# Kernel tuning notes

Hardware: AMD Instinct MI355X
Metric: run time of the kernel (lower is better)

The kernel has to match this reference:

```python
import jax, jax.numpy as jnp
import numpy as np

NUM_HEADS = 4


def setup_inputs() -> dict:
    key = jax.random.key(0)
    ks = jax.random.split(key, 5)
    B, C, L = 8, 128, 2048
    x = jax.random.normal(ks[0], (B, C, L), dtype=jnp.float32)
    # Conv1d(C, 3C, 1) == per-position linear; weight [3C, C], bias [3C]
    w_qkv = jax.random.normal(ks[1], (3 * C, C), dtype=jnp.float32) * (1.0 / np.sqrt(C))
    b_qkv = jax.random.normal(ks[2], (3 * C,), dtype=jnp.float32) * 0.01
    w_proj = jax.random.normal(ks[3], (C, C), dtype=jnp.float32) * (1.0 / np.sqrt(C))
    b_proj = jax.random.normal(ks[4], (C,), dtype=jnp.float32) * 0.01
    return {"x": x, "w_qkv": w_qkv, "b_qkv": b_qkv, "w_proj": w_proj, "b_proj": b_proj}


def reference(x, w_qkv, b_qkv, w_proj, b_proj):
    B, C, L = x.shape
    H = NUM_HEADS
    D = C // H
    scale = D ** -0.5
    # 1x1 conv qkv projection: [B, 3C, L]
    qkv = jnp.einsum('oc,bcl->bol', w_qkv, x) + b_qkv[None, :, None]
    # reshape (B,3,H,D,L) -> permute to (3,B,H,L,D)
    qkv = qkv.reshape(B, 3, H, D, L).transpose(1, 0, 2, 4, 3)
    q, k, v = qkv[0], qkv[1], qkv[2]  # each [B, H, L, D]
    attn = jax.nn.softmax(jnp.einsum('bhld,bhmd->bhlm', q, k) * scale, axis=-1)
    out = jnp.einsum('bhlm,bhmd->bhld', attn, v)  # [B, H, L, D]
    out = out.transpose(0, 1, 3, 2).reshape(B, C, L)
    out = jnp.einsum('oc,bcl->bol', w_proj, out) + b_proj[None, :, None]
    return out + x
```

## Files before the change

### kernel.cpp

```cpp
#include <hip/hip_runtime.h>

#define Bsz 8
#define Cdim 128
#define Lseq 2048
#define NH 4
#define HD 32
#define BH 32
#define QSCALE (0.17677669529663687f * 1.4426950408889634f)

typedef __bf16 bf16x8 __attribute__((ext_vector_type(8)));
typedef float f32x4 __attribute__((ext_vector_type(4)));
typedef unsigned u32x4 __attribute__((ext_vector_type(4)));

__device__ __forceinline__ float fexp2(float x) {
#if __has_builtin(__builtin_amdgcn_exp2f)
    return __builtin_amdgcn_exp2f(x);
#else
    return __expf(x * 0.6931471805599453f);
#endif
}

__device__ __forceinline__ unsigned short f2bf(float f) {
    unsigned u = __builtin_bit_cast(unsigned, f);
    u += 0x7FFFu + ((u >> 16) & 1u);
    return (unsigned short)(u >> 16);
}

__device__ __forceinline__ unsigned pack_bf16(float a, float b) {
    return (unsigned)f2bf(a) | ((unsigned)f2bf(b) << 16);
}

__device__ __forceinline__ unsigned pack_bf16_rtz(float a, float b) {
    return __builtin_amdgcn_perm(__builtin_bit_cast(unsigned, b),
                                 __builtin_bit_cast(unsigned, a), 0x07060302u);
}

__device__ __forceinline__ float bf_lo(unsigned u) {
    return __builtin_bit_cast(float, u << 16);
}
__device__ __forceinline__ float bf_hi(unsigned u) {
    return __builtin_bit_cast(float, u & 0xFFFF0000u);
}

#define MFMA16(A, B, C) __builtin_amdgcn_mfma_f32_16x16x32_bf16((A), (B), (C), 0, 0, 0)

__global__ __launch_bounds__(256) void qkv_kernel(const float* __restrict__ x,
        const float* __restrict__ w, const float* __restrict__ bias,
        unsigned short* __restrict__ qh, unsigned short* __restrict__ kh,
        unsigned short* __restrict__ vh) {
    __shared__ __attribute__((aligned(16))) unsigned short T[64][132];
    int bid = blockIdx.x;
    int og = bid % 6;
    int lt = (bid / 6) & 31;
    int b  = bid / 192;
    int l0 = lt * 64;
    int t = threadIdx.x;
    int lane = t & 63, wv = t >> 6;
    int m16 = lane & 15, quad = lane >> 4;
    int o0 = og * 64 + wv * 16;

    bf16x8 af[4];
    #pragma unroll
    for (int ks = 0; ks < 4; ks++) {
        const float* p = w + (size_t)(o0 + m16) * Cdim + ks * 32 + quad * 8;
        float4 f0 = *(const float4*)p;
        float4 f1 = *(const float4*)(p + 4);
        u32x4 u = {pack_bf16(f0.x, f0.y), pack_bf16(f0.z, f0.w),
                   pack_bf16(f1.x, f1.y), pack_bf16(f1.z, f1.w)};
        af[ks] = __builtin_bit_cast(bf16x8, u);
    }
    float bs[4];
    #pragma unroll
    for (int r = 0; r < 4; r++) bs[r] = bias[o0 + quad * 4 + r];

    {
        int ll = t & 63, cg = t >> 6;
        const float* xb = x + (size_t)b * Cdim * Lseq + l0 + ll;
        #pragma unroll
        for (int i = 0; i < 16; i++) {
            int c = cg * 32 + 2 * i;
            float f0 = xb[(size_t)c * Lseq];
            float f1 = xb[(size_t)(c + 1) * Lseq];
            *(unsigned*)&T[ll][c] = pack_bf16(f0, f1);
        }
    }
    __syncthreads();

    int oq = o0 + quad * 4;
    #pragma unroll
    for (int ns = 0; ns < 4; ns++) {
        bf16x8 bx[4];
        #pragma unroll
        for (int ks = 0; ks < 4; ks++)
            bx[ks] = *(const bf16x8*)(&T[ns * 16 + m16][ks * 32 + quad * 8]);
        f32x4 acc = {0.f, 0.f, 0.f, 0.f};
        #pragma unroll
        for (int ks = 0; ks < 4; ks++) acc = MFMA16(af[ks], bx[ks], acc);
        int l = l0 + ns * 16 + m16;
        if (og < 2) {
            int h = oq >> 5, d0 = oq & 31;
            uint2 u;
            u.x = pack_bf16((acc[0] + bs[0]) * QSCALE, (acc[1] + bs[1]) * QSCALE);
            u.y = pack_bf16((acc[2] + bs[2]) * QSCALE, (acc[3] + bs[3]) * QSCALE);
            *(uint2*)(qh + ((size_t)(b * NH + h) * Lseq + l) * HD + d0) = u;
        } else if (og < 4) {
            int o = oq - Cdim, h = o >> 5, d0 = o & 31;
            uint2 u;
            u.x = pack_bf16(acc[0] + bs[0], acc[1] + bs[1]);
            u.y = pack_bf16(acc[2] + bs[2], acc[3] + bs[3]);
            *(uint2*)(kh + ((size_t)(b * NH + h) * Lseq + l) * HD + d0) = u;
        } else {
            int kc = l >> 6, kk = l & 63;
            int half = kk >> 5, k32 = kk & 31;
            int q_, j_;
            if (k32 < 16) { q_ = k32 >> 2; j_ = k32 & 3; }
            else          { q_ = (k32 - 16) >> 2; j_ = 4 + ((k32 - 16) & 3); }
            int pos = half * 32 + q_ * 8 + j_;
            #pragma unroll
            for (int r = 0; r < 4; r++) {
                int o = oq + r - 2 * Cdim, h = o >> 5, d = o & 31;
                vh[(((size_t)(b * NH + h) * 32 + kc) * HD + d) * 64 + pos] =
                    f2bf(acc[r] + bs[r]);
            }
        }
    }
}

__global__ __launch_bounds__(256) void attn_kernel(
        const unsigned short* __restrict__ qh, const unsigned short* __restrict__ kh,
        const unsigned short* __restrict__ vh, float* __restrict__ po,
        float* __restrict__ pl) {
    __shared__ __attribute__((aligned(16))) char smem[19456];

    int bid = blockIdx.x;
    int xcd  = bid & 7;
    int rest = bid >> 3;
    int qt = rest & 31;
    int hb = rest >> 5;
    int bh = xcd + 8 * (hb & 3);
    int half = hb >> 2;

    int lane = threadIdx.x & 63;
    int wv   = threadIdx.x >> 6;
    int m16  = lane & 15;
    int quad = lane >> 4;
    int l0 = qt * 64;

    bf16x8 qf[4];
    #pragma unroll
    for (int qs = 0; qs < 4; qs++)
        qf[qs] = *(const bf16x8*)(qh + ((size_t)bh * Lseq + l0 + qs * 16 + m16) * HD + quad * 8);

    bf16x8 ones;
    #pragma unroll
    for (int i = 0; i < 8; i++) ones[i] = (__bf16)1.0f;

    f32x4 oacc[4][2];
    f32x4 lacc[4];
    #pragma unroll
    for (int qs = 0; qs < 4; qs++) {
        oacc[qs][0] = f32x4{0.f, 0.f, 0.f, 0.f};
        oacc[qs][1] = f32x4{0.f, 0.f, 0.f, 0.f};
        lacc[qs]    = f32x4{0.f, 0.f, 0.f, 0.f};
    }
    f32x4 zero = {0.f, 0.f, 0.f, 0.f};

    const unsigned short* kb = kh + (size_t)bh * Lseq * HD + m16 * HD + quad * 8;
    const unsigned short* vb = vh + (size_t)bh * 32 * HD * 64;
    int kbase = half * 1024 + wv * 256;

    auto load_kv = [&](int chunk, bf16x8* kf, bf16x8* vf) {
        int k0 = kbase + chunk * 64;
        #pragma unroll
        for (int t = 0; t < 4; t++)
            kf[t] = *(const bf16x8*)(kb + (size_t)(k0 + 16 * t) * HD);
        const unsigned short* vch = vb + (size_t)(k0 >> 6) * (HD * 64);
        vf[0] = *(const bf16x8*)(vch + m16 * 64 + quad * 8);
        vf[1] = *(const bf16x8*)(vch + (16 + m16) * 64 + quad * 8);
        vf[2] = *(const bf16x8*)(vch + m16 * 64 + 32 + quad * 8);
        vf[3] = *(const bf16x8*)(vch + (16 + m16) * 64 + 32 + quad * 8);
    };

    auto compute = [&](const bf16x8* kf, const bf16x8* vf) {
        #pragma unroll
        for (int qs = 0; qs < 4; qs++) {
            f32x4 s0 = MFMA16(kf[0], qf[qs], zero);
            f32x4 s1 = MFMA16(kf[1], qf[qs], zero);
            f32x4 s2 = MFMA16(kf[2], qf[qs], zero);
            f32x4 s3 = MFMA16(kf[3], qf[qs], zero);
            float p00 = fexp2(s0[0]), p01 = fexp2(s0[1]), p02 = fexp2(s0[2]), p03 = fexp2(s0[3]);
            float p10 = fexp2(s1[0]), p11 = fexp2(s1[1]), p12 = fexp2(s1[2]), p13 = fexp2(s1[3]);
            float p20 = fexp2(s2[0]), p21 = fexp2(s2[1]), p22 = fexp2(s2[2]), p23 = fexp2(s2[3]);
            float p30 = fexp2(s3[0]), p31 = fexp2(s3[1]), p32 = fexp2(s3[2]), p33 = fexp2(s3[3]);
            u32x4 lo = {pack_bf16_rtz(p00, p01), pack_bf16_rtz(p02, p03),
                        pack_bf16_rtz(p10, p11), pack_bf16_rtz(p12, p13)};
            u32x4 hi = {pack_bf16_rtz(p20, p21), pack_bf16_rtz(p22, p23),
                        pack_bf16_rtz(p30, p31), pack_bf16_rtz(p32, p33)};
            bf16x8 pfL = __builtin_bit_cast(bf16x8, lo);
            bf16x8 pfH = __builtin_bit_cast(bf16x8, hi);
            oacc[qs][0] = MFMA16(vf[0], pfL, oacc[qs][0]);
            oacc[qs][1] = MFMA16(vf[1], pfL, oacc[qs][1]);
            lacc[qs]    = MFMA16(ones,  pfL, lacc[qs]);
            oacc[qs][0] = MFMA16(vf[2], pfH, oacc[qs][0]);
            oacc[qs][1] = MFMA16(vf[3], pfH, oacc[qs][1]);
            lacc[qs]    = MFMA16(ones,  pfH, lacc[qs]);
        }
    };

    bf16x8 kA[4], vA[4], kB[4], vB[4];
    load_kv(0, kA, vA);
    load_kv(1, kB, vB);
    compute(kA, vA);
    load_kv(2, kA, vA);
    compute(kB, vB);
    load_kv(3, kB, vB);
    compute(kA, vA);
    compute(kB, vB);

    unsigned* red_o = (unsigned*)smem;
    float* red_l = (float*)(smem + 18432);
    #pragma unroll
    for (int qs = 0; qs < 4; qs++) {
        int row = qs * 16 + m16;
        unsigned* rw = red_o + (size_t)(wv * 64 + row) * 18;
        *(uint2*)(rw + 2 * quad) =
            make_uint2(pack_bf16_rtz(oacc[qs][0][0], oacc[qs][0][1]),
                       pack_bf16_rtz(oacc[qs][0][2], oacc[qs][0][3]));
        *(uint2*)(rw + 8 + 2 * quad) =
            make_uint2(pack_bf16_rtz(oacc[qs][1][0], oacc[qs][1][1]),
                       pack_bf16_rtz(oacc[qs][1][2], oacc[qs][1][3]));
        if (quad == 0) red_l[wv * 64 + row] = lacc[qs][0];
    }
    __syncthreads();

    int q = threadIdx.x >> 2;
    int s4 = (threadIdx.x & 3) * 4;
    float a8[8] = {0.f, 0.f, 0.f, 0.f, 0.f, 0.f, 0.f, 0.f};
    float lt = 0.f;
    #pragma unroll
    for (int w = 0; w < 4; w++) {
        const unsigned* rr = red_o + (size_t)(w * 64 + q) * 18 + s4;
        uint2 ua = *(const uint2*)(rr);
        uint2 ub = *(const uint2*)(rr + 2);
        a8[0] += bf_lo(ua.x); a8[1] += bf_hi(ua.x);
        a8[2] += bf_lo(ua.y); a8[3] += bf_hi(ua.y);
        a8[4] += bf_lo(ub.x); a8[5] += bf_hi(ub.x);
        a8[6] += bf_lo(ub.y); a8[7] += bf_hi(ub.y);
        lt += red_l[w * 64 + q];
    }
    int d0 = (threadIdx.x & 3) * 8;
    float* pob = po + ((size_t)(half * BH + bh) * Lseq + l0 + q) * HD + d0;
    *(float4*)pob       = make_float4(a8[0], a8[1], a8[2], a8[3]);
    *(float4*)(pob + 4) = make_float4(a8[4], a8[5], a8[6], a8[7]);
    if ((threadIdx.x & 3) == 0)
        pl[(size_t)(half * BH + bh) * Lseq + l0 + q] = lt;
}

__global__ __launch_bounds__(256) void proj_kernel(const float* __restrict__ wp,
        const float* __restrict__ po, const float* __restrict__ pl,
        const float* __restrict__ bias, const float* __restrict__ x,
        float* __restrict__ out) {
    __shared__ __attribute__((aligned(16))) unsigned short T[32][132];
    int bid = blockIdx.x;
    int ot = bid & 1;
    int nt = bid >> 1;
    int n0 = nt * 32;
    int t = threadIdx.x;

    {
        int nl = t >> 3, g = t & 7;
        int h = g >> 1, d0 = (g & 1) * 16;
        int n = n0 + nl, b = n >> 11, l = n & (Lseq - 1);
        int bh = b * NH + h;
        const float* p0 = po + ((size_t)bh * Lseq + l) * HD + d0;
        const float* p1 = po + ((size_t)(BH + bh) * Lseq + l) * HD + d0;
        float inv = 1.0f / (pl[(size_t)bh * Lseq + l] + pl[(size_t)(BH + bh) * Lseq + l]);
        float4 a0 = *(const float4*)p0,        a1 = *(const float4*)(p0 + 4);
        float4 a2 = *(const float4*)(p0 + 8),  a3 = *(const float4*)(p0 + 12);
        float4 b0 = *(const float4*)p1,        b1 = *(const float4*)(p1 + 4);
        float4 b2 = *(const float4*)(p1 + 8),  b3 = *(const float4*)(p1 + 12);
        uint4 u0, u1;
        u0.x = pack_bf16((a0.x + b0.x) * inv, (a0.y + b0.y) * inv);
        u0.y = pack_bf16((a0.z + b0.z) * inv, (a0.w + b0.w) * inv);
        u0.z = pack_bf16((a1.x + b1.x) * inv, (a1.y + b1.y) * inv);
        u0.w = pack_bf16((a1.z + b1.z) * inv, (a1.w + b1.w) * inv);
        u1.x = pack_bf16((a2.x + b2.x) * inv, (a2.y + b2.y) * inv);
        u1.y = pack_bf16((a2.z + b2.z) * inv, (a2.w + b2.w) * inv);
        u1.z = pack_bf16((a3.x + b3.x) * inv, (a3.y + b3.y) * inv);
        u1.w = pack_bf16((a3.z + b3.z) * inv, (a3.w + b3.w) * inv);
        int c0 = g * 16;
        *(uint4*)&T[nl][c0]     = u0;
        *(uint4*)&T[nl][c0 + 8] = u1;
    }

    int lane = t & 63;
    int wv = t >> 6;
    int m16 = lane & 15, quad = lane >> 4;
    int o0 = ot * 64 + wv * 16;

    bf16x8 af[4];
    #pragma unroll
    for (int ks = 0; ks < 4; ks++) {
        const float* p = wp + (size_t)(o0 + m16) * Cdim + ks * 32 + quad * 8;
        float4 f0 = *(const float4*)p;
        float4 f1 = *(const float4*)(p + 4);
        u32x4 u = {pack_bf16(f0.x, f0.y), pack_bf16(f0.z, f0.w),
                   pack_bf16(f1.x, f1.y), pack_bf16(f1.z, f1.w)};
        af[ks] = __builtin_bit_cast(bf16x8, u);
    }
    float bs[4];
    #pragma unroll
    for (int r = 0; r < 4; r++) bs[r] = bias[o0 + quad * 4 + r];
    int oq = o0 + quad * 4;

    __syncthreads();

    #pragma unroll
    for (int lt2 = 0; lt2 < 2; lt2++) {
        int n = n0 + lt2 * 16 + m16;
        bf16x8 bx[4];
        #pragma unroll
        for (int ks = 0; ks < 4; ks++)
            bx[ks] = *(const bf16x8*)(&T[lt2 * 16 + m16][ks * 32 + quad * 8]);
        f32x4 acc = {0.f, 0.f, 0.f, 0.f};
        #pragma unroll
        for (int ks = 0; ks < 4; ks++) acc = MFMA16(af[ks], bx[ks], acc);
        int b = n >> 11, l = n & (Lseq - 1);
        #pragma unroll
        for (int r = 0; r < 4; r++) {
            size_t xi = ((size_t)b * Cdim + oq + r) * Lseq + l;
            out[xi] = acc[r] + bs[r] + x[xi];
        }
    }
}

extern "C" void kernel_launch(void* const* d_in, const int* in_sizes, int n_in,
                              void* d_out, int out_size, void* d_ws, size_t ws_size,
                              hipStream_t stream) {
    const float* x      = (const float*)d_in[0];
    const float* w_qkv  = (const float*)d_in[1];
    const float* b_qkv  = (const float*)d_in[2];
    const float* w_proj = (const float*)d_in[3];
    const float* b_proj = (const float*)d_in[4];
    float* out = (float*)d_out;

    const size_t E = (size_t)BH * Lseq * HD;
    unsigned short* qh = (unsigned short*)d_ws;
    unsigned short* kh = qh + E;
    unsigned short* vh = kh + E;
    float* po = (float*)(vh + E);
    float* pl = po + 2 * E;

    qkv_kernel<<<dim3(1536), dim3(256), 0, stream>>>(x, w_qkv, b_qkv, qh, kh, vh);
    attn_kernel<<<dim3(2048), dim3(256), 0, stream>>>(qh, kh, vh, po, pl);
    proj_kernel<<<dim3(1024), dim3(256), 0, stream>>>(w_proj, po, pl, b_qkv == b_proj ? b_proj : b_proj, x, out);
}
```

Before: 123.2 us.

## Split attention waves 2x2 over queries and keys, store partials in bf16

```diff
diff --git a/kernel.cpp b/kernel.cpp
--- a/kernel.cpp
+++ b/kernel.cpp
@@ -126,11 +126,11 @@
     }
 }
 
-__global__ __launch_bounds__(256) void attn_kernel(
+__global__ __launch_bounds__(256, 6) void attn_kernel(
         const unsigned short* __restrict__ qh, const unsigned short* __restrict__ kh,
-        const unsigned short* __restrict__ vh, float* __restrict__ po,
+        const unsigned short* __restrict__ vh, unsigned short* __restrict__ po,
         float* __restrict__ pl) {
-    __shared__ __attribute__((aligned(16))) char smem[19456];
+    __shared__ __attribute__((aligned(16))) char smem[9728];
 
     int bid = blockIdx.x;
     int xcd  = bid & 7;
@@ -142,48 +142,46 @@
 
     int lane = threadIdx.x & 63;
     int wv   = threadIdx.x >> 6;
+    int wq   = wv >> 1;
+    int wk   = wv & 1;
     int m16  = lane & 15;
     int quad = lane >> 4;
     int l0 = qt * 64;
 
-    bf16x8 qf[4];
-    #pragma unroll
-    for (int qs = 0; qs < 4; qs++)
-        qf[qs] = *(const bf16x8*)(qh + ((size_t)bh * Lseq + l0 + qs * 16 + m16) * HD + quad * 8);
-
-    bf16x8 ones;
-    #pragma unroll
-    for (int i = 0; i < 8; i++) ones[i] = (__bf16)1.0f;
-
-    f32x4 oacc[4][2];
-    f32x4 lacc[4];
-    #pragma unroll
-    for (int qs = 0; qs < 4; qs++) {
+    bf16x8 qf[2];
+    #pragma unroll
+    for (int qs = 0; qs < 2; qs++)
+        qf[qs] = *(const bf16x8*)(qh +
+            ((size_t)bh * Lseq + l0 + wq * 32 + qs * 16 + m16) * HD + quad * 8);
+
+    f32x4 oacc[2][2];
+    #pragma unroll
+    for (int qs = 0; qs < 2; qs++) {
         oacc[qs][0] = f32x4{0.f, 0.f, 0.f, 0.f};
         oacc[qs][1] = f32x4{0.f, 0.f, 0.f, 0.f};
-        lacc[qs]    = f32x4{0.f, 0.f, 0.f, 0.f};
-    }
+    }
+    float lsum[2] = {0.f, 0.f};
     f32x4 zero = {0.f, 0.f, 0.f, 0.f};
 
     const unsigned short* kb = kh + (size_t)bh * Lseq * HD + m16 * HD + quad * 8;
     const unsigned short* vb = vh + (size_t)bh * 32 * HD * 64;
-    int kbase = half * 1024 + wv * 256;
-
-    auto load_kv = [&](int chunk, bf16x8* kf, bf16x8* vf) {
-        int k0 = kbase + chunk * 64;
+    int kbase = half * 1024 + wk * 512;
+
+    #pragma unroll 1
+    for (int it = 0; it < 8; it++) {
+        int k0 = kbase + it * 64;
+        bf16x8 kf[4];
         #pragma unroll
         for (int t = 0; t < 4; t++)
             kf[t] = *(const bf16x8*)(kb + (size_t)(k0 + 16 * t) * HD);
         const unsigned short* vch = vb + (size_t)(k0 >> 6) * (HD * 64);
-        vf[0] = *(const bf16x8*)(vch + m16 * 64 + quad * 8);
-        vf[1] = *(const bf16x8*)(vch + (16 + m16) * 64 + quad * 8);
-        vf[2] = *(const bf16x8*)(vch + m16 * 64 + 32 + quad * 8);
-        vf[3] = *(const bf16x8*)(vch + (16 + m16) * 64 + 32 + quad * 8);
-    };
-
-    auto compute = [&](const bf16x8* kf, const bf16x8* vf) {
-        #pragma unroll
-        for (int qs = 0; qs < 4; qs++) {
+        bf16x8 vf0 = *(const bf16x8*)(vch + m16 * 64 + quad * 8);
+        bf16x8 vf1 = *(const bf16x8*)(vch + (16 + m16) * 64 + quad * 8);
+        bf16x8 vf2 = *(const bf16x8*)(vch + m16 * 64 + 32 + quad * 8);
+        bf16x8 vf3 = *(const bf16x8*)(vch + (16 + m16) * 64 + 32 + quad * 8);
+
+        #pragma unroll
+        for (int qs = 0; qs < 2; qs++) {
             f32x4 s0 = MFMA16(kf[0], qf[qs], zero);
             f32x4 s1 = MFMA16(kf[1], qf[qs], zero);
             f32x4 s2 = MFMA16(kf[2], qf[qs], zero);
@@ -192,72 +190,64 @@
             float p10 = fexp2(s1[0]), p11 = fexp2(s1[1]), p12 = fexp2(s1[2]), p13 = fexp2(s1[3]);
             float p20 = fexp2(s2[0]), p21 = fexp2(s2[1]), p22 = fexp2(s2[2]), p23 = fexp2(s2[3]);
             float p30 = fexp2(s3[0]), p31 = fexp2(s3[1]), p32 = fexp2(s3[2]), p33 = fexp2(s3[3]);
+            lsum[qs] += (((p00 + p01) + (p02 + p03)) + ((p10 + p11) + (p12 + p13))) +
+                        (((p20 + p21) + (p22 + p23)) + ((p30 + p31) + (p32 + p33)));
             u32x4 lo = {pack_bf16_rtz(p00, p01), pack_bf16_rtz(p02, p03),
                         pack_bf16_rtz(p10, p11), pack_bf16_rtz(p12, p13)};
             u32x4 hi = {pack_bf16_rtz(p20, p21), pack_bf16_rtz(p22, p23),
                         pack_bf16_rtz(p30, p31), pack_bf16_rtz(p32, p33)};
             bf16x8 pfL = __builtin_bit_cast(bf16x8, lo);
             bf16x8 pfH = __builtin_bit_cast(bf16x8, hi);
-            oacc[qs][0] = MFMA16(vf[0], pfL, oacc[qs][0]);
-            oacc[qs][1] = MFMA16(vf[1], pfL, oacc[qs][1]);
-            lacc[qs]    = MFMA16(ones,  pfL, lacc[qs]);
-            oacc[qs][0] = MFMA16(vf[2], pfH, oacc[qs][0]);
-            oacc[qs][1] = MFMA16(vf[3], pfH, oacc[qs][1]);
-            lacc[qs]    = MFMA16(ones,  pfH, lacc[qs]);
+            oacc[qs][0] = MFMA16(vf0, pfL, oacc[qs][0]);
+            oacc[qs][1] = MFMA16(vf1, pfL, oacc[qs][1]);
+            oacc[qs][0] = MFMA16(vf2, pfH, oacc[qs][0]);
+            oacc[qs][1] = MFMA16(vf3, pfH, oacc[qs][1]);
         }
-    };
-
-    bf16x8 kA[4], vA[4], kB[4], vB[4];
-    load_kv(0, kA, vA);
-    load_kv(1, kB, vB);
-    compute(kA, vA);
-    load_kv(2, kA, vA);
-    compute(kB, vB);
-    load_kv(3, kB, vB);
-    compute(kA, vA);
-    compute(kB, vB);
+    }
+
+    #pragma unroll
+    for (int qs = 0; qs < 2; qs++) {
+        float v = lsum[qs];
+        v += __shfl_xor(v, 16);
+        v += __shfl_xor(v, 32);
+        lsum[qs] = v;
+    }
 
     unsigned* red_o = (unsigned*)smem;
-    float* red_l = (float*)(smem + 18432);
-    #pragma unroll
-    for (int qs = 0; qs < 4; qs++) {
-        int row = qs * 16 + m16;
-        unsigned* rw = red_o + (size_t)(wv * 64 + row) * 18;
+    float* red_l = (float*)(smem + 9216);
+    #pragma unroll
+    for (int qs = 0; qs < 2; qs++) {
+        int row = wq * 32 + qs * 16 + m16;
+        unsigned* rw = red_o + (size_t)(wk * 64 + row) * 18;
         *(uint2*)(rw + 2 * quad) =
             make_uint2(pack_bf16_rtz(oacc[qs][0][0], oacc[qs][0][1]),
                        pack_bf16_rtz(oacc[qs][0][2], oacc[qs][0][3]));
         *(uint2*)(rw + 8 + 2 * quad) =
             make_uint2(pack_bf16_rtz(oacc[qs][1][0], oacc[qs][1][1]),
                        pack_bf16_rtz(oacc[qs][1][2], oacc[qs][1][3]));
-        if (quad == 0) red_l[wv * 64 + row] = lacc[qs][0];
+        if (quad == 0) red_l[wk * 64 + row] = lsum[qs];
     }
     __syncthreads();
 
     int q = threadIdx.x >> 2;
     int s4 = (threadIdx.x & 3) * 4;
-    float a8[8] = {0.f, 0.f, 0.f, 0.f, 0.f, 0.f, 0.f, 0.f};
-    float lt = 0.f;
-    #pragma unroll
-    for (int w = 0; w < 4; w++) {
-        const unsigned* rr = red_o + (size_t)(w * 64 + q) * 18 + s4;
-        uint2 ua = *(const uint2*)(rr);
-        uint2 ub = *(const uint2*)(rr + 2);
-        a8[0] += bf_lo(ua.x); a8[1] += bf_hi(ua.x);
-        a8[2] += bf_lo(ua.y); a8[3] += bf_hi(ua.y);
-        a8[4] += bf_lo(ub.x); a8[5] += bf_hi(ub.x);
-        a8[6] += bf_lo(ub.y); a8[7] += bf_hi(ub.y);
-        lt += red_l[w * 64 + q];
-    }
+    const unsigned* r0 = red_o + (size_t)q * 18 + s4;
+    const unsigned* r1 = red_o + (size_t)(64 + q) * 18 + s4;
+    uint2 ua = *(const uint2*)r0, ub = *(const uint2*)(r0 + 2);
+    uint2 va = *(const uint2*)r1, vb2 = *(const uint2*)(r1 + 2);
+    uint4 u;
+    u.x = pack_bf16(bf_lo(ua.x) + bf_lo(va.x), bf_hi(ua.x) + bf_hi(va.x));
+    u.y = pack_bf16(bf_lo(ua.y) + bf_lo(va.y), bf_hi(ua.y) + bf_hi(va.y));
+    u.z = pack_bf16(bf_lo(ub.x) + bf_lo(vb2.x), bf_hi(ub.x) + bf_hi(vb2.x));
+    u.w = pack_bf16(bf_lo(ub.y) + bf_lo(vb2.y), bf_hi(ub.y) + bf_hi(vb2.y));
     int d0 = (threadIdx.x & 3) * 8;
-    float* pob = po + ((size_t)(half * BH + bh) * Lseq + l0 + q) * HD + d0;
-    *(float4*)pob       = make_float4(a8[0], a8[1], a8[2], a8[3]);
-    *(float4*)(pob + 4) = make_float4(a8[4], a8[5], a8[6], a8[7]);
+    *(uint4*)(po + ((size_t)(half * BH + bh) * Lseq + l0 + q) * HD + d0) = u;
     if ((threadIdx.x & 3) == 0)
-        pl[(size_t)(half * BH + bh) * Lseq + l0 + q] = lt;
+        pl[(size_t)(half * BH + bh) * Lseq + l0 + q] = red_l[q] + red_l[64 + q];
 }
 
 __global__ __launch_bounds__(256) void proj_kernel(const float* __restrict__ wp,
-        const float* __restrict__ po, const float* __restrict__ pl,
+        const unsigned short* __restrict__ po, const float* __restrict__ pl,
         const float* __restrict__ bias, const float* __restrict__ x,
         float* __restrict__ out) {
     __shared__ __attribute__((aligned(16))) unsigned short T[32][132];
@@ -272,22 +262,20 @@
         int h = g >> 1, d0 = (g & 1) * 16;
         int n = n0 + nl, b = n >> 11, l = n & (Lseq - 1);
         int bh = b * NH + h;
-        const float* p0 = po + ((size_t)bh * Lseq + l) * HD + d0;
-        const float* p1 = po + ((size_t)(BH + bh) * Lseq + l) * HD + d0;
+        const unsigned short* p0 = po + ((size_t)bh * Lseq + l) * HD + d0;
+        const unsigned short* p1 = po + ((size_t)(BH + bh) * Lseq + l) * HD + d0;
         float inv = 1.0f / (pl[(size_t)bh * Lseq + l] + pl[(size_t)(BH + bh) * Lseq + l]);
-        float4 a0 = *(const float4*)p0,        a1 = *(const float4*)(p0 + 4);
-        float4 a2 = *(const float4*)(p0 + 8),  a3 = *(const float4*)(p0 + 12);
-        float4 b0 = *(const float4*)p1,        b1 = *(const float4*)(p1 + 4);
-        float4 b2 = *(const float4*)(p1 + 8),  b3 = *(const float4*)(p1 + 12);
+        uint4 a0 = *(const uint4*)p0, a1 = *(const uint4*)(p0 + 8);
+        uint4 b0 = *(const uint4*)p1, b1 = *(const uint4*)(p1 + 8);
         uint4 u0, u1;
-        u0.x = pack_bf16((a0.x + b0.x) * inv, (a0.y + b0.y) * inv);
-        u0.y = pack_bf16((a0.z + b0.z) * inv, (a0.w + b0.w) * inv);
-        u0.z = pack_bf16((a1.x + b1.x) * inv, (a1.y + b1.y) * inv);
-        u0.w = pack_bf16((a1.z + b1.z) * inv, (a1.w + b1.w) * inv);
-        u1.x = pack_bf16((a2.x + b2.x) * inv, (a2.y + b2.y) * inv);
-        u1.y = pack_bf16((a2.z + b2.z) * inv, (a2.w + b2.w) * inv);
-        u1.z = pack_bf16((a3.x + b3.x) * inv, (a3.y + b3.y) * inv);
-        u1.w = pack_bf16((a3.z + b3.z) * inv, (a3.w + b3.w) * inv);
+        u0.x = pack_bf16((bf_lo(a0.x) + bf_lo(b0.x)) * inv, (bf_hi(a0.x) + bf_hi(b0.x)) * inv);
+        u0.y = pack_bf16((bf_lo(a0.y) + bf_lo(b0.y)) * inv, (bf_hi(a0.y) + bf_hi(b0.y)) * inv);
+        u0.z = pack_bf16((bf_lo(a0.z) + bf_lo(b0.z)) * inv, (bf_hi(a0.z) + bf_hi(b0.z)) * inv);
+        u0.w = pack_bf16((bf_lo(a0.w) + bf_lo(b0.w)) * inv, (bf_hi(a0.w) + bf_hi(b0.w)) * inv);
+        u1.x = pack_bf16((bf_lo(a1.x) + bf_lo(b1.x)) * inv, (bf_hi(a1.x) + bf_hi(b1.x)) * inv);
+        u1.y = pack_bf16((bf_lo(a1.y) + bf_lo(b1.y)) * inv, (bf_hi(a1.y) + bf_hi(b1.y)) * inv);
+        u1.z = pack_bf16((bf_lo(a1.z) + bf_lo(b1.z)) * inv, (bf_hi(a1.z) + bf_hi(b1.z)) * inv);
+        u1.w = pack_bf16((bf_lo(a1.w) + bf_lo(b1.w)) * inv, (bf_hi(a1.w) + bf_hi(b1.w)) * inv);
         int c0 = g * 16;
         *(uint4*)&T[nl][c0]     = u0;
         *(uint4*)&T[nl][c0 + 8] = u1;
@@ -348,10 +336,10 @@
     unsigned short* qh = (unsigned short*)d_ws;
     unsigned short* kh = qh + E;
     unsigned short* vh = kh + E;
-    float* po = (float*)(vh + E);
-    float* pl = po + 2 * E;
+    unsigned short* po = vh + E;
+    float* pl = (float*)(po + 2 * E);
 
     qkv_kernel<<<dim3(1536), dim3(256), 0, stream>>>(x, w_qkv, b_qkv, qh, kh, vh);
     attn_kernel<<<dim3(2048), dim3(256), 0, stream>>>(qh, kh, vh, po, pl);
-    proj_kernel<<<dim3(1024), dim3(256), 0, stream>>>(w_proj, po, pl, b_qkv == b_proj ? b_proj : b_proj, x, out);
-}
+    proj_kernel<<<dim3(1024), dim3(256), 0, stream>>>(w_proj, po, pl, b_proj, x, out);
+}
```

New measurement: 139.4 us. 13.1% more time.
